# Optimization experiments

Hardware: AMD Instinct MI355X
Metric: run time of the kernel (lower is better)

Reference implementation:

```python
import jax, jax.numpy as jnp
import numpy as np

N_ATOMS = 100000
N_MOLS = 5000
IN_F = 1008
H1, H2, H3 = 256, 192, 160
OUT_C = 1
ELEMS = np.array([1, 6, 7, 8, 9])  # H, C, N, O, F
ALPHA = 0.1


def setup_inputs() -> dict:
    key = jax.random.key(0)
    ks = jax.random.split(key, 12)
    zidx = jax.random.randint(ks[0], (N_ATOMS,), 0, 5)
    z = jnp.asarray(ELEMS)[zidx].astype(jnp.int64)
    features = jax.random.normal(ks[1], (N_ATOMS, IN_F), dtype=jnp.float32)
    batch = jnp.sort(jax.random.randint(ks[2], (N_ATOMS,), 0, N_MOLS)).astype(jnp.int64)
    # Stacked per-element MLP params: leading axis = 5 element types (H,C,N,O,F)
    def w(k, shape, fan_in):
        return jax.random.normal(k, shape, dtype=jnp.float32) / np.sqrt(fan_in)
    W1 = w(ks[3], (5, IN_F, H1), IN_F); b1 = jnp.zeros((5, H1), jnp.float32)
    W2 = w(ks[4], (5, H1, H2), H1);     b2 = jnp.zeros((5, H2), jnp.float32)
    W3 = w(ks[5], (5, H2, H3), H2);     b3 = jnp.zeros((5, H3), jnp.float32)
    W4 = w(ks[6], (5, H3, OUT_C), H3);  b4 = jnp.zeros((5, OUT_C), jnp.float32)
    return {"z": z, "features": features, "batch": batch, "n_mols": N_MOLS,
            "W1": W1, "b1": b1, "W2": W2, "b2": b2,
            "W3": W3, "b3": b3, "W4": W4, "b4": b4}


def _celu(x):
    return jax.nn.celu(x, alpha=ALPHA)


def reference(z, features, batch, n_mols, W1, b1, W2, b2, W3, b3, W4, b4):
    # Per-element-type MLPs run over all atoms (t = 5 element types), then the
    # atom's true type is selected via a one-hot mask -- equivalent to the
    # gather -> per-type MLP -> scatter-back in the torch forward.
    h = _celu(jnp.einsum('nf,tfh->tnh', features, W1) + b1[:, None, :])
    h = _celu(jnp.einsum('tnh,thg->tng', h, W2) + b2[:, None, :])
    h = _celu(jnp.einsum('tng,tgk->tnk', h, W3) + b3[:, None, :])
    v_all = jnp.einsum('tnk,tko->tno', h, W4) + b4[:, None, :]  # [5, N, out]
    onehot = (z[None, :] == jnp.asarray(ELEMS)[:, None]).astype(features.dtype)  # [5, N]
    v = jnp.einsum('tn,tno->no', onehot, v_all)  # [N, out]
    u = jax.ops.segment_sum(v, batch, num_segments=n_mols)  # [n_mols, out]
    return u
```

## Files before the change

### kernel.cpp

```cpp
#include <hip/hip_runtime.h>
#include <stdint.h>

#define NF    1008
#define KP1   1024
#define NH1   256
#define NH2   192
#define NH3   160
#define MT    64
#define CELU_ALPHA 0.1f

typedef __attribute__((ext_vector_type(8))) __bf16 bf16x8;
typedef __attribute__((ext_vector_type(4))) float  f32x4;

#define W1T_OFF   0u
#define W2T_OFF   2621440u
#define W3T_OFF   3112960u
#define META_OFF  3420160u
#define SORT_OFF  3420288u

__device__ __forceinline__ unsigned short f2bf(float f) {
  union { float f; uint32_t u; } v; v.f = f;
  uint32_t u = v.u;
  uint32_t r = u + 0x7FFFu + ((u >> 16) & 1u);
  return (unsigned short)(r >> 16);
}

__device__ __forceinline__ float celu_f(float x) {
  return x > 0.f ? x : CELU_ALPHA * (__expf(x * (1.f / CELU_ALPHA)) - 1.f);
}

__device__ __forceinline__ int ztype(int z) {
  return z == 1 ? 0 : z == 6 ? 1 : z == 7 ? 2 : z == 8 ? 3 : 4;
}

__global__ void prep_and_hist(const float* __restrict__ W1, const float* __restrict__ W2,
                              const float* __restrict__ W3,
                              unsigned short* __restrict__ w1t, unsigned short* __restrict__ w2t,
                              unsigned short* __restrict__ w3t,
                              const int* __restrict__ z, int n, int* __restrict__ counts) {
  int bid = blockIdx.x;
  int tid = threadIdx.x;
  if (bid >= 425) {
    __shared__ int h[5];
    if (tid < 5) h[tid] = 0;
    __syncthreads();
    int i = (bid - 425) * 256 + tid;
    if (i < n) atomicAdd(&h[ztype(z[i])], 1);
    __syncthreads();
    if (tid < 5 && h[tid]) atomicAdd(&counts[tid], h[tid]);
    return;
  }
  const float* src; unsigned short* dst; int K, N, KP, kt, nt;
  if (bid < 320) {
    int t = bid / 64, r = bid % 64; kt = r / 4; nt = r % 4;
    src = W1 + (size_t)t * NF * NH1; dst = w1t + (size_t)t * NH1 * KP1;
    K = NF; N = NH1; KP = KP1;
  } else if (bid < 380) {
    int b = bid - 320; int t = b / 12, r = b % 12; kt = r / 3; nt = r % 3;
    src = W2 + (size_t)t * NH1 * NH2; dst = w2t + (size_t)t * NH2 * NH1;
    K = NH1; N = NH2; KP = NH1;
  } else {
    int b = bid - 380; int t = b / 9, r = b % 9; kt = r / 3; nt = r % 3;
    src = W3 + (size_t)t * NH2 * NH3; dst = w3t + (size_t)t * NH3 * NH2;
    K = NH2; N = NH3; KP = NH2;
  }
  __shared__ float tile[64][65];
  int k0 = kt * 64, n0 = nt * 64;
  {
    int nl = tid & 63, kb = tid >> 6;
    #pragma unroll
    for (int i = 0; i < 16; ++i) {
      int kl = kb + 4 * i;
      int k = k0 + kl, nn = n0 + nl;
      tile[kl][nl] = (k < K && nn < N) ? src[(size_t)k * N + nn] : 0.f;
    }
  }
  __syncthreads();
  {
    int klw = tid & 63, nb2 = tid >> 6;
    #pragma unroll
    for (int i = 0; i < 16; ++i) {
      int nl = nb2 + 4 * i;
      int nn = n0 + nl, k = k0 + klw;
      if (nn < N && k < KP) dst[(size_t)nn * KP + k] = f2bf(tile[klw][nl]);
    }
  }
}

__global__ void plan_tiles(const int* __restrict__ counts, int* __restrict__ atom_base,
                           int* __restrict__ tile_base) {
  if (threadIdx.x == 0 && blockIdx.x == 0) {
    int a = 0, tb = 0;
    for (int t = 0; t < 5; ++t) {
      atom_base[t] = a; tile_base[t] = tb;
      a += counts[t]; tb += (counts[t] + MT - 1) / MT;
    }
    atom_base[5] = a; tile_base[5] = tb;
  }
}

__global__ void scatter_atoms(const int* __restrict__ z, int n,
                              const int* __restrict__ atom_base, int* __restrict__ cursors,
                              int* __restrict__ sorted) {
  int i = blockIdx.x * blockDim.x + threadIdx.x;
  int lane = threadIdx.x & 63;
  int t = (i < n) ? ztype(z[i]) : -1;
  #pragma unroll
  for (int tt = 0; tt < 5; ++tt) {
    unsigned long long mask = __ballot(t == tt);
    if (t == tt) {
      int leader = __ffsll((long long)mask) - 1;
      int rank = __popcll(mask & ((1ull << lane) - 1ull));
      int base = 0;
      if (lane == leader) base = atomicAdd(&cursors[tt], (int)__popcll(mask));
      base = __shfl(base, leader);
      sorted[atom_base[tt] + base + rank] = i;
    }
  }
}

__global__ __launch_bounds__(512, 4) void fcnn_main(
    const float* __restrict__ feat, const int* __restrict__ batch,
    const unsigned short* __restrict__ w1t, const unsigned short* __restrict__ w2t,
    const unsigned short* __restrict__ w3t, const float* __restrict__ W4,
    const float* __restrict__ b1, const float* __restrict__ b2,
    const float* __restrict__ b3, const float* __restrict__ b4,
    const int* __restrict__ atom_base, const int* __restrict__ tile_base,
    const int* __restrict__ sorted_idx, float* __restrict__ out) {
  __shared__ __align__(16) unsigned char smem[67840];
  unsigned short* A0  = (unsigned short*)smem;
  unsigned short* A1  = (unsigned short*)(smem + 33792);
  unsigned short* h1s = (unsigned short*)smem;
  unsigned short* h2s = (unsigned short*)(smem + 33792);
  unsigned short* h3s = (unsigned short*)smem;
  int* lgid = (int*)(smem + 67584);

  const int bid = blockIdx.x;
  if (bid >= tile_base[5]) return;
  int t = 0;
  #pragma unroll
  for (int i = 0; i < 4; ++i) if (bid >= tile_base[i + 1]) t = i + 1;
  const int m0 = atom_base[t] + (bid - tile_base[t]) * MT;
  const int rows = min(MT, atom_base[t + 1] - m0);

  const int tid = threadIdx.x;
  const int lane = tid & 63;
  const int w = tid >> 6;
  const int col = lane & 15;
  const int q = lane >> 4;

  if (tid < MT) lgid[tid] = (tid < rows) ? sorted_idx[m0 + tid] : -1;
  __syncthreads();

  const int srow = tid >> 3;
  const int sl = tid & 7;
  const int sg = lgid[srow];
  const float* fsrc = (sg >= 0) ? (feat + (size_t)sg * NF) : feat;
  const unsigned short* w1p = w1t + (size_t)t * NH1 * KP1;

  f32x4 acc[4][2];
  #pragma unroll
  for (int a = 0; a < 4; ++a)
    #pragma unroll
    for (int b = 0; b < 2; ++b) acc[a][b] = (f32x4){0.f, 0.f, 0.f, 0.f};

  f32x4 nv[8];
  #pragma unroll
  for (int i = 0; i < 8; ++i) {
    int k = (sl + 8 * i) * 4;
    nv[i] = (sg >= 0 && k < NF) ? *(const f32x4*)(fsrc + k) : (f32x4){0.f, 0.f, 0.f, 0.f};
  }
  #pragma unroll
  for (int i = 0; i < 8; ++i) {
    int c = sl + 8 * i;
    ushort4 pk;
    pk.x = f2bf(nv[i][0]); pk.y = f2bf(nv[i][1]); pk.z = f2bf(nv[i][2]); pk.w = f2bf(nv[i][3]);
    *(ushort4*)(A0 + srow * 264 + c * 4) = pk;
  }
  __syncthreads();

  #pragma unroll 1
  for (int kc = 0; kc < 4; ++kc) {
    if (kc < 3) {
      #pragma unroll
      for (int i = 0; i < 8; ++i) {
        int k = (kc + 1) * 256 + (sl + 8 * i) * 4;
        nv[i] = (sg >= 0 && k < NF) ? *(const f32x4*)(fsrc + k) : (f32x4){0.f, 0.f, 0.f, 0.f};
      }
    }
    const unsigned short* ab = (kc & 1) ? A1 : A0;
    #pragma unroll
    for (int ks = 0; ks < 8; ++ks) {
      bf16x8 af[4];
      #pragma unroll
      for (int im = 0; im < 4; ++im)
        af[im] = *(const bf16x8*)(ab + (im * 16 + col) * 264 + ks * 32 + q * 8);
      #pragma unroll
      for (int jj = 0; jj < 2; ++jj) {
        int n = (w + 8 * jj) * 16 + col;
        bf16x8 bfr = *(const bf16x8*)(w1p + (size_t)n * KP1 + kc * 256 + ks * 32 + q * 8);
        #pragma unroll
        for (int im = 0; im < 4; ++im)
          acc[im][jj] = __builtin_amdgcn_mfma_f32_16x16x32_bf16(af[im], bfr, acc[im][jj], 0, 0, 0);
      }
    }
    if (kc < 3) {
      unsigned short* dst = (kc & 1) ? A0 : A1;
      #pragma unroll
      for (int i = 0; i < 8; ++i) {
        int c = sl + 8 * i;
        ushort4 pk;
        pk.x = f2bf(nv[i][0]); pk.y = f2bf(nv[i][1]); pk.z = f2bf(nv[i][2]); pk.w = f2bf(nv[i][3]);
        *(ushort4*)(dst + srow * 264 + c * 4) = pk;
      }
    }
    __syncthreads();
  }

  #pragma unroll
  for (int jj = 0; jj < 2; ++jj) {
    int n = (w + 8 * jj) * 16 + col;
    float bias = b1[t * NH1 + n];
    #pragma unroll
    for (int im = 0; im < 4; ++im)
      #pragma unroll
      for (int r = 0; r < 4; ++r)
        h1s[(im * 16 + q * 4 + r) * 264 + n] = f2bf(celu_f(acc[im][jj][r] + bias));
  }
  __syncthreads();

  f32x4 acc2[4][2];
  #pragma unroll
  for (int a = 0; a < 4; ++a)
    #pragma unroll
    for (int b = 0; b < 2; ++b) acc2[a][b] = (f32x4){0.f, 0.f, 0.f, 0.f};
  const unsigned short* w2p = w2t + (size_t)t * NH2 * NH1;
  #pragma unroll
  for (int ks = 0; ks < 8; ++ks) {
    bf16x8 af[4];
    #pragma unroll
    for (int im = 0; im < 4; ++im)
      af[im] = *(const bf16x8*)(h1s + (im * 16 + col) * 264 + ks * 32 + q * 8);
    #pragma unroll
    for (int jj = 0; jj < 2; ++jj) {
      int j = w + 8 * jj;
      if (j < 12) {
        int n = j * 16 + col;
        bf16x8 bfr = *(const bf16x8*)(w2p + (size_t)n * NH1 + ks * 32 + q * 8);
        #pragma unroll
        for (int im = 0; im < 4; ++im)
          acc2[im][jj] = __builtin_amdgcn_mfma_f32_16x16x32_bf16(af[im], bfr, acc2[im][jj], 0, 0, 0);
      }
    }
  }
  #pragma unroll
  for (int jj = 0; jj < 2; ++jj) {
    int j = w + 8 * jj;
    if (j < 12) {
      int n = j * 16 + col;
      float bias = b2[t * NH2 + n];
      #pragma unroll
      for (int im = 0; im < 4; ++im)
        #pragma unroll
        for (int r = 0; r < 4; ++r)
          h2s[(im * 16 + q * 4 + r) * 200 + n] = f2bf(celu_f(acc2[im][jj][r] + bias));
    }
  }
  __syncthreads();

  f32x4 acc3[4][2];
  #pragma unroll
  for (int a = 0; a < 4; ++a)
    #pragma unroll
    for (int b = 0; b < 2; ++b) acc3[a][b] = (f32x4){0.f, 0.f, 0.f, 0.f};
  const unsigned short* w3p = w3t + (size_t)t * NH3 * NH2;
  #pragma unroll
  for (int ks = 0; ks < 6; ++ks) {
    bf16x8 af[4];
    #pragma unroll
    for (int im = 0; im < 4; ++im)
      af[im] = *(const bf16x8*)(h2s + (im * 16 + col) * 200 + ks * 32 + q * 8);
    #pragma unroll
    for (int jj = 0; jj < 2; ++jj) {
      int j = w + 8 * jj;
      if (j < 10) {
        int n = j * 16 + col;
        bf16x8 bfr = *(const bf16x8*)(w3p + (size_t)n * NH2 + ks * 32 + q * 8);
        #pragma unroll
        for (int im = 0; im < 4; ++im)
          acc3[im][jj] = __builtin_amdgcn_mfma_f32_16x16x32_bf16(af[im], bfr, acc3[im][jj], 0, 0, 0);
      }
    }
  }
  #pragma unroll
  for (int jj = 0; jj < 2; ++jj) {
    int j = w + 8 * jj;
    if (j < 10) {
      int n = j * 16 + col;
      float bias = b3[t * NH3 + n];
      #pragma unroll
      for (int im = 0; im < 4; ++im)
        #pragma unroll
        for (int r = 0; r < 4; ++r)
          h3s[(im * 16 + q * 4 + r) * 168 + n] = f2bf(celu_f(acc3[im][jj][r] + bias));
    }
  }
  __syncthreads();

  {
    int a = tid >> 3, p = tid & 7;
    float v = 0.f;
    if (a < rows) {
      const float* wp = W4 + t * NH3;
      #pragma unroll
      for (int c0 = 0; c0 < 3; ++c0) {
        int c = p + 8 * c0;
        if (c < 20) {
          bf16x8 hv = *(const bf16x8*)(h3s + a * 168 + c * 8);
          #pragma unroll
          for (int j = 0; j < 8; ++j) v += (float)hv[j] * wp[c * 8 + j];
        }
      }
    }
    v += __shfl_xor(v, 1);
    v += __shfl_xor(v, 2);
    v += __shfl_xor(v, 4);
    if (p == 0 && a < rows) {
      int g = lgid[a];
      atomicAdd(&out[batch[g]], v + b4[t]);
    }
  }
}

extern "C" void kernel_launch(void* const* d_in, const int* in_sizes, int n_in,
                              void* d_out, int out_size, void* d_ws, size_t ws_size,
                              hipStream_t stream) {
  const int*   z    = (const int*)d_in[0];
  const float* feat = (const float*)d_in[1];
  const int*   bat  = (const int*)d_in[2];
  const float* W1 = (const float*)d_in[4];
  const float* b1 = (const float*)d_in[5];
  const float* W2 = (const float*)d_in[6];
  const float* b2 = (const float*)d_in[7];
  const float* W3 = (const float*)d_in[8];
  const float* b3 = (const float*)d_in[9];
  const float* W4 = (const float*)d_in[10];
  const float* b4 = (const float*)d_in[11];
  const int n = in_sizes[0];

  unsigned char* ws = (unsigned char*)d_ws;
  unsigned short* w1t = (unsigned short*)(ws + W1T_OFF);
  unsigned short* w2t = (unsigned short*)(ws + W2T_OFF);
  unsigned short* w3t = (unsigned short*)(ws + W3T_OFF);
  int* meta = (int*)(ws + META_OFF);
  int* counts    = meta;
  int* atom_base = meta + 8;
  int* tile_base = meta + 16;
  int* cursors   = meta + 24;
  int* sorted    = (int*)(ws + SORT_OFF);

  hipMemsetAsync(meta, 0, 128, stream);
  hipMemsetAsync(d_out, 0, (size_t)out_size * sizeof(float), stream);

  int nb = (n + 255) / 256;
  prep_and_hist<<<425 + nb, 256, 0, stream>>>(W1, W2, W3, w1t, w2t, w3t, z, n, counts);
  plan_tiles<<<1, 64, 0, stream>>>(counts, atom_base, tile_base);
  scatter_atoms<<<nb, 256, 0, stream>>>(z, n, atom_base, cursors, sorted);
  int max_tiles = n / MT + 6;
  fcnn_main<<<max_tiles, 512, 0, stream>>>(feat, bat, w1t, w2t, w3t, W4,
                                           b1, b2, b3, b4,
                                           atom_base, tile_base, sorted,
                                           (float*)d_out);
  (void)n_in; (void)ws_size;
}
```

Baseline: 784.2 us.

## Pre-swizzle weights into MFMA fragment order and XOR-swizzle LDS activations

Weights are now stored in MFMA B-fragment order, so each lane's 16-byte fragment load is contiguous and fully coalesced instead of strided across rows of K. LDS activation tiles drop their row padding and use an XOR swizzle to avoid bank conflicts, which shrinks shared memory use. The per-layer loops are simplified to two explicit fragment pointers with warp-guarded second tiles. Indexing is more intricate, and a mistake in any swizzle mapping would produce wrong results.

```diff
diff --git a/kernel.cpp b/kernel.cpp
--- a/kernel.cpp
+++ b/kernel.cpp
@@ -2,7 +2,6 @@
 #include <stdint.h>
 
 #define NF    1008
-#define KP1   1024
 #define NH1   256
 #define NH2   192
 #define NH3   160
@@ -12,9 +11,9 @@
 typedef __attribute__((ext_vector_type(8))) __bf16 bf16x8;
 typedef __attribute__((ext_vector_type(4))) float  f32x4;
 
-#define W1T_OFF   0u
-#define W2T_OFF   2621440u
-#define W3T_OFF   3112960u
+#define W1F_OFF   0u
+#define W2F_OFF   2621440u
+#define W3F_OFF   3112960u
 #define META_OFF  3420160u
 #define SORT_OFF  3420288u
 
@@ -35,8 +34,8 @@
 
 __global__ void prep_and_hist(const float* __restrict__ W1, const float* __restrict__ W2,
                               const float* __restrict__ W3,
-                              unsigned short* __restrict__ w1t, unsigned short* __restrict__ w2t,
-                              unsigned short* __restrict__ w3t,
+                              unsigned short* __restrict__ w1f, unsigned short* __restrict__ w2f,
+                              unsigned short* __restrict__ w3f,
                               const int* __restrict__ z, int n, int* __restrict__ counts) {
   int bid = blockIdx.x;
   int tid = threadIdx.x;
@@ -50,19 +49,19 @@
     if (tid < 5 && h[tid]) atomicAdd(&counts[tid], h[tid]);
     return;
   }
-  const float* src; unsigned short* dst; int K, N, KP, kt, nt;
+  const float* src; unsigned short* dst; int K, N, NJ, NKS, kt, nt;
   if (bid < 320) {
     int t = bid / 64, r = bid % 64; kt = r / 4; nt = r % 4;
-    src = W1 + (size_t)t * NF * NH1; dst = w1t + (size_t)t * NH1 * KP1;
-    K = NF; N = NH1; KP = KP1;
+    src = W1 + (size_t)t * NF * NH1; dst = w1f + (size_t)t * 16 * 32 * 512;
+    K = NF; N = NH1; NJ = 16; NKS = 32;
   } else if (bid < 380) {
     int b = bid - 320; int t = b / 12, r = b % 12; kt = r / 3; nt = r % 3;
-    src = W2 + (size_t)t * NH1 * NH2; dst = w2t + (size_t)t * NH2 * NH1;
-    K = NH1; N = NH2; KP = NH1;
+    src = W2 + (size_t)t * NH1 * NH2; dst = w2f + (size_t)t * 12 * 8 * 512;
+    K = NH1; N = NH2; NJ = 12; NKS = 8;
   } else {
     int b = bid - 380; int t = b / 9, r = b % 9; kt = r / 3; nt = r % 3;
-    src = W3 + (size_t)t * NH2 * NH3; dst = w3t + (size_t)t * NH3 * NH2;
-    K = NH2; N = NH3; KP = NH2;
+    src = W3 + (size_t)t * NH2 * NH3; dst = w3f + (size_t)t * 10 * 6 * 512;
+    K = NH2; N = NH3; NJ = 10; NKS = 6;
   }
   __shared__ float tile[64][65];
   int k0 = kt * 64, n0 = nt * 64;
@@ -77,12 +76,19 @@
   }
   __syncthreads();
   {
-    int klw = tid & 63, nb2 = tid >> 6;
     #pragma unroll
     for (int i = 0; i < 16; ++i) {
-      int nl = nb2 + 4 * i;
-      int nn = n0 + nl, k = k0 + klw;
-      if (nn < N && k < KP) dst[(size_t)nn * KP + k] = f2bf(tile[klw][nl]);
+      int o = tid + 256 * i;
+      int e  = o & 7;
+      int l  = (o >> 3) & 63;
+      int ks2 = (o >> 9) & 1;
+      int j2  = o >> 10;
+      int kl = ks2 * 32 + ((l >> 4) << 3) + e;
+      int nl = j2 * 16 + (l & 15);
+      int gj  = (n0 >> 4) + j2;
+      int gks = (k0 >> 5) + ks2;
+      if (gj < NJ && gks < NKS)
+        dst[((size_t)gj * NKS + gks) * 512 + (o & 511)] = f2bf(tile[kl][nl]);
     }
   }
 }
@@ -121,19 +127,19 @@
 
 __global__ __launch_bounds__(512, 4) void fcnn_main(
     const float* __restrict__ feat, const int* __restrict__ batch,
-    const unsigned short* __restrict__ w1t, const unsigned short* __restrict__ w2t,
-    const unsigned short* __restrict__ w3t, const float* __restrict__ W4,
+    const unsigned short* __restrict__ w1f, const unsigned short* __restrict__ w2f,
+    const unsigned short* __restrict__ w3f, const float* __restrict__ W4,
     const float* __restrict__ b1, const float* __restrict__ b2,
     const float* __restrict__ b3, const float* __restrict__ b4,
     const int* __restrict__ atom_base, const int* __restrict__ tile_base,
     const int* __restrict__ sorted_idx, float* __restrict__ out) {
-  __shared__ __align__(16) unsigned char smem[67840];
+  __shared__ __align__(16) unsigned char smem[65792];
   unsigned short* A0  = (unsigned short*)smem;
-  unsigned short* A1  = (unsigned short*)(smem + 33792);
+  unsigned short* A1  = (unsigned short*)(smem + 32768);
   unsigned short* h1s = (unsigned short*)smem;
-  unsigned short* h2s = (unsigned short*)(smem + 33792);
+  unsigned short* h2s = (unsigned short*)(smem + 32768);
   unsigned short* h3s = (unsigned short*)smem;
-  int* lgid = (int*)(smem + 67584);
+  int* lgid = (int*)(smem + 65536);
 
   const int bid = blockIdx.x;
   if (bid >= tile_base[5]) return;
@@ -148,6 +154,8 @@
   const int w = tid >> 6;
   const int col = lane & 15;
   const int q = lane >> 4;
+  const int lx8 = lane << 3;
+  const int swzR = (col & 7) << 3;
 
   if (tid < MT) lgid[tid] = (tid < rows) ? sorted_idx[m0 + tid] : -1;
   __syncthreads();
@@ -156,7 +164,10 @@
   const int sl = tid & 7;
   const int sg = lgid[srow];
   const float* fsrc = (sg >= 0) ? (feat + (size_t)sg * NF) : feat;
-  const unsigned short* w1p = w1t + (size_t)t * NH1 * KP1;
+  const int swzW = (srow & 7) << 3;
+
+  const unsigned short* w1p0 = w1f + (size_t)t * 16 * 32 * 512 + (size_t)w * 32 * 512 + lx8;
+  const unsigned short* w1p1 = w1p0 + 8 * 32 * 512;
 
   f32x4 acc[4][2];
   #pragma unroll
@@ -175,7 +186,7 @@
     int c = sl + 8 * i;
     ushort4 pk;
     pk.x = f2bf(nv[i][0]); pk.y = f2bf(nv[i][1]); pk.z = f2bf(nv[i][2]); pk.w = f2bf(nv[i][3]);
-    *(ushort4*)(A0 + srow * 264 + c * 4) = pk;
+    *(ushort4*)(A0 + srow * 256 + (((c << 2)) ^ swzW)) = pk;
   }
   __syncthreads();
 
@@ -194,14 +205,13 @@
       bf16x8 af[4];
       #pragma unroll
       for (int im = 0; im < 4; ++im)
-        af[im] = *(const bf16x8*)(ab + (im * 16 + col) * 264 + ks * 32 + q * 8);
-      #pragma unroll
-      for (int jj = 0; jj < 2; ++jj) {
-        int n = (w + 8 * jj) * 16 + col;
-        bf16x8 bfr = *(const bf16x8*)(w1p + (size_t)n * KP1 + kc * 256 + ks * 32 + q * 8);
-        #pragma unroll
-        for (int im = 0; im < 4; ++im)
-          acc[im][jj] = __builtin_amdgcn_mfma_f32_16x16x32_bf16(af[im], bfr, acc[im][jj], 0, 0, 0);
+        af[im] = *(const bf16x8*)(ab + (im * 16 + col) * 256 + ((ks * 32 + q * 8) ^ swzR));
+      bf16x8 bf0 = *(const bf16x8*)(w1p0 + (size_t)(kc * 8 + ks) * 512);
+      bf16x8 bf1 = *(const bf16x8*)(w1p1 + (size_t)(kc * 8 + ks) * 512);
+      #pragma unroll
+      for (int im = 0; im < 4; ++im) {
+        acc[im][0] = __builtin_amdgcn_mfma_f32_16x16x32_bf16(af[im], bf0, acc[im][0], 0, 0, 0);
+        acc[im][1] = __builtin_amdgcn_mfma_f32_16x16x32_bf16(af[im], bf1, acc[im][1], 0, 0, 0);
       }
     }
     if (kc < 3) {
@@ -211,7 +221,7 @@
         int c = sl + 8 * i;
         ushort4 pk;
         pk.x = f2bf(nv[i][0]); pk.y = f2bf(nv[i][1]); pk.z = f2bf(nv[i][2]); pk.w = f2bf(nv[i][3]);
-        *(ushort4*)(dst + srow * 264 + c * 4) = pk;
+        *(ushort4*)(dst + srow * 256 + (((c << 2)) ^ swzW)) = pk;
       }
     }
     __syncthreads();
@@ -224,8 +234,10 @@
     #pragma unroll
     for (int im = 0; im < 4; ++im)
       #pragma unroll
-      for (int r = 0; r < 4; ++r)
-        h1s[(im * 16 + q * 4 + r) * 264 + n] = f2bf(celu_f(acc[im][jj][r] + bias));
+      for (int r = 0; r < 4; ++r) {
+        int row = im * 16 + q * 4 + r;
+        h1s[row * 256 + (n ^ ((row & 7) << 3))] = f2bf(celu_f(acc[im][jj][r] + bias));
+      }
   }
   __syncthreads();
 
@@ -234,23 +246,23 @@
   for (int a = 0; a < 4; ++a)
     #pragma unroll
     for (int b = 0; b < 2; ++b) acc2[a][b] = (f32x4){0.f, 0.f, 0.f, 0.f};
-  const unsigned short* w2p = w2t + (size_t)t * NH2 * NH1;
+  const unsigned short* w2p0 = w2f + (size_t)t * 12 * 8 * 512 + (size_t)w * 8 * 512 + lx8;
+  const unsigned short* w2p1 = w2p0 + 8 * 8 * 512;
   #pragma unroll
   for (int ks = 0; ks < 8; ++ks) {
     bf16x8 af[4];
     #pragma unroll
     for (int im = 0; im < 4; ++im)
-      af[im] = *(const bf16x8*)(h1s + (im * 16 + col) * 264 + ks * 32 + q * 8);
-    #pragma unroll
-    for (int jj = 0; jj < 2; ++jj) {
-      int j = w + 8 * jj;
-      if (j < 12) {
-        int n = j * 16 + col;
-        bf16x8 bfr = *(const bf16x8*)(w2p + (size_t)n * NH1 + ks * 32 + q * 8);
-        #pragma unroll
-        for (int im = 0; im < 4; ++im)
-          acc2[im][jj] = __builtin_amdgcn_mfma_f32_16x16x32_bf16(af[im], bfr, acc2[im][jj], 0, 0, 0);
-      }
+      af[im] = *(const bf16x8*)(h1s + (im * 16 + col) * 256 + ((ks * 32 + q * 8) ^ swzR));
+    bf16x8 bf0 = *(const bf16x8*)(w2p0 + (size_t)ks * 512);
+    #pragma unroll
+    for (int im = 0; im < 4; ++im)
+      acc2[im][0] = __builtin_amdgcn_mfma_f32_16x16x32_bf16(af[im], bf0, acc2[im][0], 0, 0, 0);
+    if (w < 4) {
+      bf16x8 bf1 = *(const bf16x8*)(w2p1 + (size_t)ks * 512);
+      #pragma unroll
+      for (int im = 0; im < 4; ++im)
+        acc2[im][1] = __builtin_amdgcn_mfma_f32_16x16x32_bf16(af[im], bf1, acc2[im][1], 0, 0, 0);
     }
   }
   #pragma unroll
@@ -262,8 +274,10 @@
       #pragma unroll
       for (int im = 0; im < 4; ++im)
         #pragma unroll
-        for (int r = 0; r < 4; ++r)
-          h2s[(im * 16 + q * 4 + r) * 200 + n] = f2bf(celu_f(acc2[im][jj][r] + bias));
+        for (int r = 0; r < 4; ++r) {
+          int row = im * 16 + q * 4 + r;
+          h2s[row * 192 + (n ^ ((row & 7) << 3))] = f2bf(celu_f(acc2[im][jj][r] + bias));
+        }
     }
   }
   __syncthreads();
@@ -273,23 +287,23 @@
   for (int a = 0; a < 4; ++a)
     #pragma unroll
     for (int b = 0; b < 2; ++b) acc3[a][b] = (f32x4){0.f, 0.f, 0.f, 0.f};
-  const unsigned short* w3p = w3t + (size_t)t * NH3 * NH2;
+  const unsigned short* w3p0 = w3f + (size_t)t * 10 * 6 * 512 + (size_t)w * 6 * 512 + lx8;
+  const unsigned short* w3p1 = w3p0 + 8 * 6 * 512;
   #pragma unroll
   for (int ks = 0; ks < 6; ++ks) {
     bf16x8 af[4];
     #pragma unroll
     for (int im = 0; im < 4; ++im)
-      af[im] = *(const bf16x8*)(h2s + (im * 16 + col) * 200 + ks * 32 + q * 8);
-    #pragma unroll
-    for (int jj = 0; jj < 2; ++jj) {
-      int j = w + 8 * jj;
-      if (j < 10) {
-        int n = j * 16 + col;
-        bf16x8 bfr = *(const bf16x8*)(w3p + (size_t)n * NH2 + ks * 32 + q * 8);
-        #pragma unroll
-        for (int im = 0; im < 4; ++im)
-          acc3[im][jj] = __builtin_amdgcn_mfma_f32_16x16x32_bf16(af[im], bfr, acc3[im][jj], 0, 0, 0);
-      }
+      af[im] = *(const bf16x8*)(h2s + (im * 16 + col) * 192 + ((ks * 32 + q * 8) ^ swzR));
+    bf16x8 bf0 = *(const bf16x8*)(w3p0 + (size_t)ks * 512);
+    #pragma unroll
+    for (int im = 0; im < 4; ++im)
+      acc3[im][0] = __builtin_amdgcn_mfma_f32_16x16x32_bf16(af[im], bf0, acc3[im][0], 0, 0, 0);
+    if (w < 2) {
+      bf16x8 bf1 = *(const bf16x8*)(w3p1 + (size_t)ks * 512);
+      #pragma unroll
+      for (int im = 0; im < 4; ++im)
+        acc3[im][1] = __builtin_amdgcn_mfma_f32_16x16x32_bf16(af[im], bf1, acc3[im][1], 0, 0, 0);
     }
   }
   #pragma unroll
@@ -301,8 +315,10 @@
       #pragma unroll
       for (int im = 0; im < 4; ++im)
         #pragma unroll
-        for (int r = 0; r < 4; ++r)
-          h3s[(im * 16 + q * 4 + r) * 168 + n] = f2bf(celu_f(acc3[im][jj][r] + bias));
+        for (int r = 0; r < 4; ++r) {
+          int row = im * 16 + q * 4 + r;
+          h3s[row * 192 + (n ^ ((row & 7) << 3))] = f2bf(celu_f(acc3[im][jj][r] + bias));
+        }
     }
   }
   __syncthreads();
@@ -312,11 +328,12 @@
     float v = 0.f;
     if (a < rows) {
       const float* wp = W4 + t * NH3;
+      int aswz = (a & 7) << 3;
       #pragma unroll
       for (int c0 = 0; c0 < 3; ++c0) {
         int c = p + 8 * c0;
         if (c < 20) {
-          bf16x8 hv = *(const bf16x8*)(h3s + a * 168 + c * 8);
+          bf16x8 hv = *(const bf16x8*)(h3s + a * 192 + ((c * 8) ^ aswz));
           #pragma unroll
           for (int j = 0; j < 8; ++j) v += (float)hv[j] * wp[c * 8 + j];
         }
@@ -349,9 +366,9 @@
   const int n = in_sizes[0];
 
   unsigned char* ws = (unsigned char*)d_ws;
-  unsigned short* w1t = (unsigned short*)(ws + W1T_OFF);
-  unsigned short* w2t = (unsigned short*)(ws + W2T_OFF);
-  unsigned short* w3t = (unsigned short*)(ws + W3T_OFF);
+  unsigned short* w1f = (unsigned short*)(ws + W1F_OFF);
+  unsigned short* w2f = (unsigned short*)(ws + W2F_OFF);
+  unsigned short* w3f = (unsigned short*)(ws + W3F_OFF);
   int* meta = (int*)(ws + META_OFF);
   int* counts    = meta;
   int* atom_base = meta + 8;
@@ -363,11 +380,11 @@
   hipMemsetAsync(d_out, 0, (size_t)out_size * sizeof(float), stream);
 
   int nb = (n + 255) / 256;
-  prep_and_hist<<<425 + nb, 256, 0, stream>>>(W1, W2, W3, w1t, w2t, w3t, z, n, counts);
+  prep_and_hist<<<425 + nb, 256, 0, stream>>>(W1, W2, W3, w1f, w2f, w3f, z, n, counts);
   plan_tiles<<<1, 64, 0, stream>>>(counts, atom_base, tile_base);
   scatter_atoms<<<nb, 256, 0, stream>>>(z, n, atom_base, cursors, sorted);
   int max_tiles = n / MT + 6;
-  fcnn_main<<<max_tiles, 512, 0, stream>>>(feat, bat, w1t, w2t, w3t, W4,
+  fcnn_main<<<max_tiles, 512, 0, stream>>>(feat, bat, w1f, w2f, w3f, W4,
                                            b1, b2, b3, b4,
                                            atom_base, tile_base, sorted,
                                            (float*)d_out);
```

After: 740.2 us. 1.06x faster.
